# Kernel optimization log

Measured on AMD Instinct MI355X. Metric: run time of the kernel, lower is better.

## Reference

```python
import jax, jax.numpy as jnp
import numpy as np


def setup_inputs() -> dict:
    key = jax.random.key(0)
    k1, k2 = jax.random.split(key)
    mat_1 = jax.random.normal(k1, (8192, 128), dtype=jnp.float32)
    mat_2 = jax.random.normal(k2, (8192, 128), dtype=jnp.float32)
    return {"mat_1": mat_1, "mat_2": mat_2}


def reference(mat_1, mat_2):
    # Squared Euclidean distance between every row of mat_1 and every row of mat_2.
    # Same math as sum((mat_1[i] - mat_2[j])**2) but expressed via the
    # ||a||^2 + ||b||^2 - 2 a.b identity so the [n1, n2, d] intermediate is
    # never materialized (single GEMM + rank-1 broadcasts).
    sq1 = jnp.sum(mat_1 * mat_1, axis=1, keepdims=True)        # [n1, 1]
    sq2 = jnp.sum(mat_2 * mat_2, axis=1)                        # [n2]
    cross = jnp.einsum('id,jd->ij', mat_1, mat_2)               # [n1, n2]
    return sq1 + sq2[None, :] - 2.0 * cross
```

## Files before the change

kernel.cpp:

```cpp
#include <hip/hip_runtime.h>
#include <hip/hip_bf16.h>


typedef __attribute__((ext_vector_type(8))) short bf16x8;
typedef __attribute__((ext_vector_type(4))) float f32x4;

__global__ void norms_kernel(const float* __restrict__ m1,
                             const float* __restrict__ m2,
                             float* __restrict__ n1,
                             float* __restrict__ n2,
                             int rows1, int rows2) {
    int gwave = (int)((blockIdx.x * blockDim.x + threadIdx.x) >> 6);
    int lane  = threadIdx.x & 63;
    const float* src;
    float* dst;
    int row;
    if (gwave < rows1) { src = m1; dst = n1; row = gwave; }
    else {
        row = gwave - rows1;
        if (row >= rows2) return;
        src = m2; dst = n2;
    }
    const float2* p = (const float2*)(src + (size_t)row * 128);
    float2 v = p[lane];
    float s = v.x * v.x + v.y * v.y;
#pragma unroll
    for (int off = 32; off; off >>= 1) s += __shfl_xor(s, off, 64);
    if (lane == 0) dst[row] = s;
}

#define BM 128
#define BN 128

__device__ __forceinline__ bf16x8 cvt8(float4 v0, float4 v1) {
    union { bf16x8 v; __hip_bfloat162 h[4]; } u;
    u.h[0] = __float22bfloat162_rn(make_float2(v0.x, v0.y));
    u.h[1] = __float22bfloat162_rn(make_float2(v0.z, v0.w));
    u.h[2] = __float22bfloat162_rn(make_float2(v1.x, v1.y));
    u.h[3] = __float22bfloat162_rn(make_float2(v1.z, v1.w));
    return u.v;
}

__global__ __launch_bounds__(256, 2)
void dist_kernel(const float* __restrict__ A, const float* __restrict__ B,
                 const float* __restrict__ n1, const float* __restrict__ n2,
                 float* __restrict__ out, int N2) {
    __shared__ char lds[65536];

    const int tid  = threadIdx.x;
    const int wave = tid >> 6;
    const int lane = tid & 63;
    const int q    = lane >> 4;
    const int l15  = lane & 15;

    const int ti = blockIdx.y * BM;
    const int tj = blockIdx.x * BN;

#pragma unroll
    for (int g = 0; g < 8; ++g) {
        int idx = tid + g * 256;
        int row = idx >> 4;
        int ke  = (idx & 15) * 8;
        int sw  = (ke * 2) ^ ((row & 7) << 4);
        const float4* pa = (const float4*)(A + (size_t)(ti + row) * 128 + ke);
        *(bf16x8*)(lds + row * 256 + sw) = cvt8(pa[0], pa[1]);
    }
#pragma unroll
    for (int g = 0; g < 8; ++g) {
        int idx = tid + g * 256;
        int row = idx >> 4;
        int ke  = (idx & 15) * 8;
        int sw  = (ke * 2) ^ ((row & 7) << 4);
        const float4* pb = (const float4*)(B + (size_t)(tj + row) * 128 + ke);
        *(bf16x8*)(lds + 32768 + row * 256 + sw) = cvt8(pb[0], pb[1]);
    }
    __syncthreads();

    const int wm = (wave >> 1) * 64;
    const int wn = (wave & 1) * 64;

    f32x4 acc[4][4] = {};

    const char* Abase = lds;
    const char* Bbase = lds + 32768;
#pragma unroll
    for (int kk = 0; kk < 128; kk += 32) {
        const int cb = kk * 2 + q * 16;
        bf16x8 af[4], bfr[4];
#pragma unroll
        for (int mi = 0; mi < 4; ++mi) {
            int row = wm + mi * 16 + l15;
            af[mi] = *(const bf16x8*)(Abase + row * 256 + (cb ^ ((row & 7) << 4)));
        }
#pragma unroll
        for (int ni = 0; ni < 4; ++ni) {
            int row = wn + ni * 16 + l15;
            bfr[ni] = *(const bf16x8*)(Bbase + row * 256 + (cb ^ ((row & 7) << 4)));
        }
#pragma unroll
        for (int mi = 0; mi < 4; ++mi)
#pragma unroll
            for (int ni = 0; ni < 4; ++ni)
                acc[mi][ni] = __builtin_amdgcn_mfma_f32_16x16x32_bf16(
                    af[mi], bfr[ni], acc[mi][ni], 0, 0, 0);
    }

#pragma unroll
    for (int mi = 0; mi < 4; ++mi) {
        int r0 = ti + wm + mi * 16 + q * 4;
        float a0 = n1[r0 + 0], a1 = n1[r0 + 1], a2 = n1[r0 + 2], a3 = n1[r0 + 3];
#pragma unroll
        for (int ni = 0; ni < 4; ++ni) {
            int c = tj + wn + ni * 16 + l15;
            float nb = n2[c];
            f32x4 v = acc[mi][ni];
            out[(size_t)(r0 + 0) * N2 + c] = a0 + nb - 2.0f * v[0];
            out[(size_t)(r0 + 1) * N2 + c] = a1 + nb - 2.0f * v[1];
            out[(size_t)(r0 + 2) * N2 + c] = a2 + nb - 2.0f * v[2];
            out[(size_t)(r0 + 3) * N2 + c] = a3 + nb - 2.0f * v[3];
        }
    }
}

extern "C" void kernel_launch(void* const* d_in, const int* in_sizes, int n_in,
                              void* d_out, int out_size, void* d_ws, size_t ws_size,
                              hipStream_t stream) {
    const float* m1 = (const float*)d_in[0];
    const float* m2 = (const float*)d_in[1];
    float* out = (float*)d_out;
    const int rows1 = in_sizes[0] / 128;
    const int rows2 = in_sizes[1] / 128;

    float* n1 = (float*)d_ws;
    float* n2 = n1 + rows1;

    int total_waves = rows1 + rows2;
    int nb = (total_waves * 64 + 255) / 256;
    norms_kernel<<<nb, 256, 0, stream>>>(m1, m2, n1, n2, rows1, rows2);

    dim3 grid(rows2 / BN, rows1 / BM);
    dist_kernel<<<grid, 256, 0, stream>>>(m1, m2, n1, n2, out, rows2);
}
```

Before: 276.7 us.

## Fuse row norms into distance kernel and stage output via LDS for coalesced stores

Drops the separate norms kernel. Each block now computes the squared norms of its A and B tiles while loading and converting them, reduces them with lane shuffles, and keeps them in LDS. The epilogue writes results into LDS (reusing the operand space) and then emits full-row 16-byte nontemporal stores instead of scattered 4-byte stores. This removes one launch and the global norm traffic, and the output write is the dominant cost. In exchange it adds redundant norm work per tile, extra barriers, and slightly more LDS, which may affect occupancy.

```diff
diff --git a/kernel.cpp b/kernel.cpp
--- a/kernel.cpp
+++ b/kernel.cpp
@@ -4,30 +4,6 @@
 
 typedef __attribute__((ext_vector_type(8))) short bf16x8;
 typedef __attribute__((ext_vector_type(4))) float f32x4;
-
-__global__ void norms_kernel(const float* __restrict__ m1,
-                             const float* __restrict__ m2,
-                             float* __restrict__ n1,
-                             float* __restrict__ n2,
-                             int rows1, int rows2) {
-    int gwave = (int)((blockIdx.x * blockDim.x + threadIdx.x) >> 6);
-    int lane  = threadIdx.x & 63;
-    const float* src;
-    float* dst;
-    int row;
-    if (gwave < rows1) { src = m1; dst = n1; row = gwave; }
-    else {
-        row = gwave - rows1;
-        if (row >= rows2) return;
-        src = m2; dst = n2;
-    }
-    const float2* p = (const float2*)(src + (size_t)row * 128);
-    float2 v = p[lane];
-    float s = v.x * v.x + v.y * v.y;
-#pragma unroll
-    for (int off = 32; off; off >>= 1) s += __shfl_xor(s, off, 64);
-    if (lane == 0) dst[row] = s;
-}
 
 #define BM 128
 #define BN 128
@@ -43,9 +19,10 @@
 
 __global__ __launch_bounds__(256, 2)
 void dist_kernel(const float* __restrict__ A, const float* __restrict__ B,
-                 const float* __restrict__ n1, const float* __restrict__ n2,
                  float* __restrict__ out, int N2) {
-    __shared__ char lds[65536];
+    __shared__ char lds[66560];
+    float* nA = (float*)(lds + 65536);
+    float* nB = (float*)(lds + 66048);
 
     const int tid  = threadIdx.x;
     const int wave = tid >> 6;
@@ -63,7 +40,13 @@
         int ke  = (idx & 15) * 8;
         int sw  = (ke * 2) ^ ((row & 7) << 4);
         const float4* pa = (const float4*)(A + (size_t)(ti + row) * 128 + ke);
-        *(bf16x8*)(lds + row * 256 + sw) = cvt8(pa[0], pa[1]);
+        float4 v0 = pa[0], v1 = pa[1];
+        *(bf16x8*)(lds + row * 256 + sw) = cvt8(v0, v1);
+        float s = v0.x*v0.x + v0.y*v0.y + v0.z*v0.z + v0.w*v0.w
+                + v1.x*v1.x + v1.y*v1.y + v1.z*v1.z + v1.w*v1.w;
+        s += __shfl_xor(s, 1); s += __shfl_xor(s, 2);
+        s += __shfl_xor(s, 4); s += __shfl_xor(s, 8);
+        if ((idx & 15) == 0) nA[row] = s;
     }
 #pragma unroll
     for (int g = 0; g < 8; ++g) {
@@ -72,7 +55,13 @@
         int ke  = (idx & 15) * 8;
         int sw  = (ke * 2) ^ ((row & 7) << 4);
         const float4* pb = (const float4*)(B + (size_t)(tj + row) * 128 + ke);
-        *(bf16x8*)(lds + 32768 + row * 256 + sw) = cvt8(pb[0], pb[1]);
+        float4 v0 = pb[0], v1 = pb[1];
+        *(bf16x8*)(lds + 32768 + row * 256 + sw) = cvt8(v0, v1);
+        float s = v0.x*v0.x + v0.y*v0.y + v0.z*v0.z + v0.w*v0.w
+                + v1.x*v1.x + v1.y*v1.y + v1.z*v1.z + v1.w*v1.w;
+        s += __shfl_xor(s, 1); s += __shfl_xor(s, 2);
+        s += __shfl_xor(s, 4); s += __shfl_xor(s, 8);
+        if ((idx & 15) == 0) nB[row] = s;
     }
     __syncthreads();
 
@@ -105,20 +94,42 @@
                     af[mi], bfr[ni], acc[mi][ni], 0, 0, 0);
     }
 
+    float an[4][4], bn[4];
 #pragma unroll
     for (int mi = 0; mi < 4; ++mi) {
-        int r0 = ti + wm + mi * 16 + q * 4;
-        float a0 = n1[r0 + 0], a1 = n1[r0 + 1], a2 = n1[r0 + 2], a3 = n1[r0 + 3];
+        float4 t = *(const float4*)&nA[wm + mi * 16 + q * 4];
+        an[mi][0] = t.x; an[mi][1] = t.y; an[mi][2] = t.z; an[mi][3] = t.w;
+    }
+#pragma unroll
+    for (int ni = 0; ni < 4; ++ni) bn[ni] = nB[wn + ni * 16 + l15];
+
+    __syncthreads();
+
+#pragma unroll
+    for (int mi = 0; mi < 4; ++mi) {
 #pragma unroll
         for (int ni = 0; ni < 4; ++ni) {
-            int c = tj + wn + ni * 16 + l15;
-            float nb = n2[c];
+            int c = wn + ni * 16 + l15;
             f32x4 v = acc[mi][ni];
-            out[(size_t)(r0 + 0) * N2 + c] = a0 + nb - 2.0f * v[0];
-            out[(size_t)(r0 + 1) * N2 + c] = a1 + nb - 2.0f * v[1];
-            out[(size_t)(r0 + 2) * N2 + c] = a2 + nb - 2.0f * v[2];
-            out[(size_t)(r0 + 3) * N2 + c] = a3 + nb - 2.0f * v[3];
+#pragma unroll
+            for (int j = 0; j < 4; ++j) {
+                int row = wm + mi * 16 + q * 4 + j;
+                *(float*)(lds + row * 512 + ((c * 4) ^ (((row >> 2) & 1) << 6)))
+                    = an[mi][j] + bn[ni] - 2.0f * v[j];
+            }
         }
+    }
+    __syncthreads();
+
+    const int l31 = lane & 31;
+    const int h   = lane >> 5;
+#pragma unroll
+    for (int p = 0; p < 16; ++p) {
+        int row = wave * 32 + p * 2 + h;
+        int cb  = (l31 * 16) ^ (((row >> 2) & 1) << 6);
+        f32x4 v = *(const f32x4*)(lds + row * 512 + cb);
+        __builtin_nontemporal_store(
+            v, (f32x4*)(out + (size_t)(ti + row) * N2 + tj + l31 * 4));
     }
 }
 
@@ -131,13 +142,6 @@
     const int rows1 = in_sizes[0] / 128;
     const int rows2 = in_sizes[1] / 128;
 
-    float* n1 = (float*)d_ws;
-    float* n2 = n1 + rows1;
-
-    int total_waves = rows1 + rows2;
-    int nb = (total_waves * 64 + 255) / 256;
-    norms_kernel<<<nb, 256, 0, stream>>>(m1, m2, n1, n2, rows1, rows2);
-
     dim3 grid(rows2 / BN, rows1 / BM);
-    dist_kernel<<<grid, 256, 0, stream>>>(m1, m2, n1, n2, out, rows2);
+    dist_kernel<<<grid, 256, 0, stream>>>(m1, m2, out, rows2);
 }
```

After: 340.3 us. +23.0%, slower.
